# Kernel optimization log

Measured on AMD Instinct MI355X. Metric: run time of the kernel, lower is better.

Reference implementation:

```python
import jax, jax.numpy as jnp
import numpy as np

B, L, D, H, E, K = 1, 512, 512, 512, 32, 2

def setup_inputs() -> dict:
    key = jax.random.key(0)
    ks = jax.random.split(key, 6)
    x = jax.random.normal(ks[0], (B, L, D), dtype=jnp.float32)
    router_scale = 1.0 + 0.02 * jax.random.normal(ks[1], (D,), dtype=jnp.float32)
    router_logits_w = 0.02 * jax.random.normal(ks[2], (D, E), dtype=jnp.float32)
    gating_einsum = 0.02 * jax.random.normal(ks[3], (E, 2, H, D), dtype=jnp.float32)
    linear_w = 0.02 * jax.random.normal(ks[4], (E, H, D), dtype=jnp.float32)
    per_expert_scale = 1.0 + 0.02 * jax.random.normal(ks[5], (E,), dtype=jnp.float32)
    return {"x": x, "router_scale": router_scale, "router_logits_w": router_logits_w,
            "gating_einsum": gating_einsum, "linear_w": linear_w,
            "per_expert_scale": per_expert_scale}

def reference(x, router_scale, router_logits_w, gating_einsum, linear_w, per_expert_scale):
    d = x.shape[-1]
    n_experts = router_logits_w.shape[-1]
    # RMSNorm without scale (fp32)
    x32 = x.astype(jnp.float32)
    var = jnp.mean(jnp.square(x32), axis=-1, keepdims=True)
    router_input = x32 * jax.lax.rsqrt(var + 1e-6)
    root_size = jax.lax.rsqrt(jnp.asarray(d, dtype=router_input.dtype))
    router_input = router_input * root_size * router_scale.astype(router_input.dtype)
    logits = jnp.dot(router_input, router_logits_w).astype(jnp.float32)  # [B,L,E]
    probs = jax.nn.softmax(logits, axis=-1)
    _, top_k_indices = jax.lax.top_k(logits, K)  # [B,L,K]
    indicator = jax.nn.one_hot(top_k_indices, n_experts, dtype=probs.dtype).sum(axis=-2)
    gate_weights = indicator * probs
    renorm = jnp.sum(gate_weights, axis=-1, keepdims=True)
    renorm = jnp.where(renorm > 0.0, renorm, 1.0)
    weights = probs / renorm
    top_k_weights = jnp.take_along_axis(weights, top_k_indices, axis=-1)  # [B,L,K]
    output = jnp.zeros_like(x)
    for ki in range(K):  # small fixed k; faithful to source's per-slot gather
        expert_idx = top_k_indices[:, :, ki]          # [B,L] int32
        expert_w = top_k_weights[:, :, ki]            # [B,L]
        gate_params = gating_einsum[expert_idx]       # [B,L,2,H,D] -- the big gather
        lin_params = linear_w[expert_idx]             # [B,L,H,D]
        escale = per_expert_scale[expert_idx]         # [B,L]
        gate_0 = jnp.einsum('bld,blhd->blh', x, gate_params[:, :, 0])
        gate_1 = jnp.einsum('bld,blhd->blh', x, gate_params[:, :, 1])
        activated = jax.nn.gelu(gate_0) * gate_1
        expert_out = jnp.einsum('blh,blhd->bld', activated, lin_params)
        output = output + expert_out * (escale * expert_w)[..., None]
    return output
```

## Files before the change

### kernel.cpp

```cpp
#include <hip/hip_runtime.h>
#include <hip/hip_bf16.h>
#include <math.h>

#define LTOK 512
#define DDIM 512
#define NEXP 32
#define HDIM 512

typedef __attribute__((ext_vector_type(8))) short short8;
typedef __attribute__((ext_vector_type(4))) float floatx4;

__device__ __forceinline__ unsigned bpack(float a, float b) {
    unsigned ua = __float_as_uint(a), ub = __float_as_uint(b);
    ua += 0x7FFFu + ((ua >> 16) & 1u);
    ub += 0x7FFFu + ((ub >> 16) & 1u);
    return (ua >> 16) | (ub & 0xFFFF0000u);
}


__global__ __launch_bounds__(64) void router_kernel(
    const float* __restrict__ x, const float* __restrict__ rs,
    const float* __restrict__ Wr, const float* __restrict__ pes,
    int* __restrict__ cnt, int* __restrict__ alist, float* __restrict__ slist,
    short* __restrict__ xb)
{
    const int t = blockIdx.x;
    const int lane = threadIdx.x;

    float xv[8];
    float ss = 0.f;
#pragma unroll
    for (int j = 0; j < 8; ++j) {
        xv[j] = x[t * DDIM + j * 64 + lane];
        ss += xv[j] * xv[j];
    }
#pragma unroll
    for (int j = 0; j < 8; ++j)
        xb[t * DDIM + j * 64 + lane] = (short)(bpack(xv[j], 0.f) & 0xFFFFu);

#pragma unroll
    for (int o = 32; o > 0; o >>= 1) ss += __shfl_xor(ss, o);
    const float var = ss * (1.0f / 512.0f);
    const float coef = rsqrtf(var + 1e-6f) * rsqrtf(512.0f);

    __shared__ float ri[DDIM];
#pragma unroll
    for (int j = 0; j < 8; ++j) {
        const int d = j * 64 + lane;
        ri[d] = xv[j] * coef * rs[d];
    }
    __syncthreads();

    const int e = lane & 31;
    const int half = lane >> 5;
    const int dbeg = half * 256;
    float l0 = 0.f, l1 = 0.f, l2 = 0.f, l3 = 0.f;
#pragma unroll 4
    for (int d = dbeg; d < dbeg + 256; d += 4) {
        l0 = fmaf(ri[d + 0], Wr[(d + 0) * NEXP + e], l0);
        l1 = fmaf(ri[d + 1], Wr[(d + 1) * NEXP + e], l1);
        l2 = fmaf(ri[d + 2], Wr[(d + 2) * NEXP + e], l2);
        l3 = fmaf(ri[d + 3], Wr[(d + 3) * NEXP + e], l3);
    }
    float lg = (l0 + l1) + (l2 + l3);
    lg += __shfl_xor(lg, 32);

    __shared__ float lgs[NEXP];
    if (lane < 32) lgs[lane] = lg;
    __syncthreads();

    if (lane == 0) {
        int i0 = 0; float m0 = lgs[0];
        for (int i = 1; i < NEXP; ++i) if (lgs[i] > m0) { m0 = lgs[i]; i0 = i; }
        int i1 = -1; float m1 = -1e30f;
        for (int i = 0; i < NEXP; ++i) if (i != i0 && lgs[i] > m1) { m1 = lgs[i]; i1 = i; }
        const float e1 = expf(m1 - m0);
        const float inv = 1.0f / (1.0f + e1);
        const float w0 = inv, w1 = e1 * inv;

        int p0 = atomicAdd(&cnt[i0], 1);
        alist[i0 * LTOK + p0] = t * 2;
        slist[i0 * LTOK + p0] = w0 * pes[i0];
        int p1 = atomicAdd(&cnt[i1], 1);
        alist[i1 * LTOK + p1] = t * 2 + 1;
        slist[i1 * LTOK + p1] = w1 * pes[i1];
    }
}

__global__ __launch_bounds__(256, 4) void gates_kernel(
    const short* __restrict__ xb, const float* __restrict__ G,
    const int* __restrict__ cnt, const int* __restrict__ alist,
    short* __restrict__ act)
{
    const int e  = blockIdx.y;
    const int h0 = blockIdx.x * 16;
    const int Ne = cnt[e];
    if (Ne == 0) return;
    const int wv   = threadIdx.x >> 6;
    const int g    = wv & 1;
    const int kh   = wv >> 1;
    const int lane = threadIdx.x & 63;
    const int n    = lane & 15;
    const int quad = lane >> 4;

    __shared__ float red[4][4][4][64];

    const float* Grow = G + ((size_t)((e * 2 + g) * HDIM) + h0 + n) * DDIM + kh * 256;
    const short* xbh  = xb + kh * 256;
    const int* al = alist + e * LTOK;

    for (int mb = 0; mb < Ne; mb += 64) {
        int arow[4];
#pragma unroll
        for (int i = 0; i < 4; ++i) {
            int s = mb + i * 16 + n;
            arow[i] = al[s < Ne ? s : Ne - 1] >> 1;
        }
        floatx4 acc[4] = {};

#pragma unroll 4
        for (int ks = 0; ks < 8; ++ks) {
            const int ko = ks * 32 + quad * 8;
            const floatx4 b0 = *(const floatx4*)(Grow + ko);
            const floatx4 b1 = *(const floatx4*)(Grow + ko + 4);
            union { short8 s; unsigned u[4]; } B;
            B.u[0] = bpack(b0.x, b0.y);
            B.u[1] = bpack(b0.z, b0.w);
            B.u[2] = bpack(b1.x, b1.y);
            B.u[3] = bpack(b1.z, b1.w);
#pragma unroll
            for (int i = 0; i < 4; ++i) {
                const short8 A = *(const short8*)(xbh + (size_t)arow[i] * DDIM + ko);
                acc[i] = __builtin_amdgcn_mfma_f32_16x16x32_bf16(A, B.s, acc[i], 0, 0, 0);
            }
        }

#pragma unroll
        for (int i = 0; i < 4; ++i)
#pragma unroll
            for (int r = 0; r < 4; ++r)
                red[wv][i][r][lane] = acc[i][r];
        __syncthreads();

        {
            const int i = wv;
#pragma unroll
            for (int r = 0; r < 4; ++r) {
                const int s = mb + i * 16 + quad * 4 + r;
                if (s < Ne) {
                    const int a = al[s];
                    const float g0 = red[0][i][r][lane] + red[2][i][r][lane];
                    const float g1 = red[1][i][r][lane] + red[3][i][r][lane];
                    const float u = 0.7978845608f * (g0 + 0.044715f * g0 * g0 * g0);
                    const float sg = 1.0f / (1.0f + __expf(-2.0f * u));
                    const float v = g0 * sg * g1;
                    act[(size_t)a * HDIM + h0 + n] = (short)(bpack(v, 0.f) & 0xFFFFu);
                }
            }
        }
        __syncthreads();
    }
}

__global__ __launch_bounds__(256, 4) void linear_kernel(
    const short* __restrict__ act, const float* __restrict__ Wl,
    const int* __restrict__ cnt, const int* __restrict__ alist,
    const float* __restrict__ slist, float* __restrict__ out)
{
    const int e  = blockIdx.y;
    const int d0 = blockIdx.x * 16;
    const int Ne = cnt[e];
    if (Ne == 0) return;
    const int wv   = threadIdx.x >> 6;
    const int lane = threadIdx.x & 63;
    const int n    = lane & 15;
    const int quad = lane >> 4;

    __shared__ float red[4][4][4][64];

    const float* Wcol = Wl + (size_t)e * HDIM * DDIM + d0 + n;
    const int* al = alist + e * LTOK;
    const float* sl = slist + e * LTOK;

    for (int mb = 0; mb < Ne; mb += 64) {
        int arow[4];
#pragma unroll
        for (int i = 0; i < 4; ++i) {
            int s = mb + i * 16 + n;
            arow[i] = al[s < Ne ? s : Ne - 1];
        }
        floatx4 acc[4] = {};

#pragma unroll 2
        for (int ks = 0; ks < 4; ++ks) {
            const int ko = wv * 128 + ks * 32 + quad * 8;
            float w[8];
#pragma unroll
            for (int j = 0; j < 8; ++j)
                w[j] = Wcol[(size_t)(ko + j) * DDIM];
            union { short8 s; unsigned u[4]; } B;
            B.u[0] = bpack(w[0], w[1]);
            B.u[1] = bpack(w[2], w[3]);
            B.u[2] = bpack(w[4], w[5]);
            B.u[3] = bpack(w[6], w[7]);
#pragma unroll
            for (int i = 0; i < 4; ++i) {
                const short8 A = *(const short8*)(act + (size_t)arow[i] * HDIM + ko);
                acc[i] = __builtin_amdgcn_mfma_f32_16x16x32_bf16(A, B.s, acc[i], 0, 0, 0);
            }
        }

#pragma unroll
        for (int i = 0; i < 4; ++i)
#pragma unroll
            for (int r = 0; r < 4; ++r)
                red[wv][i][r][lane] = acc[i][r];
        __syncthreads();

        {
            const int i = wv;
#pragma unroll
            for (int r = 0; r < 4; ++r) {
                const int s = mb + i * 16 + quad * 4 + r;
                if (s < Ne) {
                    const int a = al[s];
                    const float v = ((red[0][i][r][lane] + red[1][i][r][lane]) +
                                     (red[2][i][r][lane] + red[3][i][r][lane])) * sl[s];
                    atomicAdd(&out[(size_t)(a >> 1) * DDIM + d0 + n], v);
                }
            }
        }
        __syncthreads();
    }
}

extern "C" void kernel_launch(void* const* d_in, const int* in_sizes, int n_in,
                              void* d_out, int out_size, void* d_ws, size_t ws_size,
                              hipStream_t stream)
{
    const float* x   = (const float*)d_in[0];
    const float* rs  = (const float*)d_in[1];
    const float* Wr  = (const float*)d_in[2];
    const float* G   = (const float*)d_in[3];
    const float* Wl  = (const float*)d_in[4];
    const float* pes = (const float*)d_in[5];
    float* out = (float*)d_out;

    char* ws = (char*)d_ws;
    int*   cnt   = (int*)(ws);
    int*   alist = (int*)(ws + 256);
    float* slist = (float*)(ws + 256 + 65536);
    short* xb    = (short*)(ws + 131328);
    short* act   = (short*)(ws + 655616);

    hipMemsetAsync(cnt, 0, NEXP * sizeof(int), stream);
    hipMemsetAsync(out, 0, (size_t)out_size * sizeof(float), stream);

    router_kernel<<<dim3(LTOK), dim3(64), 0, stream>>>(x, rs, Wr, pes, cnt, alist, slist, xb);
    gates_kernel<<<dim3(32, NEXP), dim3(256), 0, stream>>>(xb, G, cnt, alist, act);
    linear_kernel<<<dim3(32, NEXP), dim3(256), 0, stream>>>(act, Wl, cnt, alist, slist, out);
}
```

Before: 165.4 us.

## Hoist expert weight fragments into registers and replace atomics with combine kernel

Both expert GEMM kernels now load and convert their bf16 weight fragments once, before the token loop, and keep them in registers across all token tiles instead of reloading them per tile. The token tile shrinks from 64 to 32 rows to keep register use down. The linear kernel writes each (token, slot) result to a scratch buffer rather than doing atomicAdd into the output, and a new combine kernel sums the two slots per token. This drops the output memset and atomic contention, at the cost of an extra launch and extra scratch traffic.

```diff
diff --git a/kernel.cpp b/kernel.cpp
--- a/kernel.cpp
+++ b/kernel.cpp
@@ -103,56 +103,65 @@
     const int n    = lane & 15;
     const int quad = lane >> 4;
 
-    __shared__ float red[4][4][4][64];
+    __shared__ float red[4][2][4][64];
 
     const float* Grow = G + ((size_t)((e * 2 + g) * HDIM) + h0 + n) * DDIM + kh * 256;
     const short* xbh  = xb + kh * 256;
     const int* al = alist + e * LTOK;
 
-    for (int mb = 0; mb < Ne; mb += 64) {
-        int arow[4];
-#pragma unroll
-        for (int i = 0; i < 4; ++i) {
+    short8 Bf[8];
+#pragma unroll
+    for (int ks = 0; ks < 8; ++ks) {
+        const int ko = ks * 32 + quad * 8;
+        const floatx4 b0 = *(const floatx4*)(Grow + ko);
+        const floatx4 b1 = *(const floatx4*)(Grow + ko + 4);
+        union { short8 s; unsigned u[4]; } B;
+        B.u[0] = bpack(b0.x, b0.y);
+        B.u[1] = bpack(b0.z, b0.w);
+        B.u[2] = bpack(b1.x, b1.y);
+        B.u[3] = bpack(b1.z, b1.w);
+        Bf[ks] = B.s;
+    }
+
+    for (int mb = 0; mb < Ne; mb += 32) {
+        int arow[2];
+#pragma unroll
+        for (int i = 0; i < 2; ++i) {
             int s = mb + i * 16 + n;
             arow[i] = al[s < Ne ? s : Ne - 1] >> 1;
         }
-        floatx4 acc[4] = {};
-
-#pragma unroll 4
+        floatx4 acc[2] = {};
+
+#pragma unroll
         for (int ks = 0; ks < 8; ++ks) {
             const int ko = ks * 32 + quad * 8;
-            const floatx4 b0 = *(const floatx4*)(Grow + ko);
-            const floatx4 b1 = *(const floatx4*)(Grow + ko + 4);
-            union { short8 s; unsigned u[4]; } B;
-            B.u[0] = bpack(b0.x, b0.y);
-            B.u[1] = bpack(b0.z, b0.w);
-            B.u[2] = bpack(b1.x, b1.y);
-            B.u[3] = bpack(b1.z, b1.w);
-#pragma unroll
-            for (int i = 0; i < 4; ++i) {
+#pragma unroll
+            for (int i = 0; i < 2; ++i) {
                 const short8 A = *(const short8*)(xbh + (size_t)arow[i] * DDIM + ko);
-                acc[i] = __builtin_amdgcn_mfma_f32_16x16x32_bf16(A, B.s, acc[i], 0, 0, 0);
-            }
-        }
-
-#pragma unroll
-        for (int i = 0; i < 4; ++i)
+                acc[i] = __builtin_amdgcn_mfma_f32_16x16x32_bf16(A, Bf[ks], acc[i], 0, 0, 0);
+            }
+        }
+
+#pragma unroll
+        for (int i = 0; i < 2; ++i)
 #pragma unroll
             for (int r = 0; r < 4; ++r)
                 red[wv][i][r][lane] = acc[i][r];
         __syncthreads();
 
         {
-            const int i = wv;
-#pragma unroll
-            for (int r = 0; r < 4; ++r) {
+            const int i = wv & 1;
+            const int u = wv >> 1;
+#pragma unroll
+            for (int rr = 0; rr < 2; ++rr) {
+                const int r = u * 2 + rr;
                 const int s = mb + i * 16 + quad * 4 + r;
                 if (s < Ne) {
                     const int a = al[s];
                     const float g0 = red[0][i][r][lane] + red[2][i][r][lane];
                     const float g1 = red[1][i][r][lane] + red[3][i][r][lane];
-                    const float u = 0.7978845608f * (g0 + 0.044715f * g0 * g0 * g0);
-                    const float sg = 1.0f / (1.0f + __expf(-2.0f * u));
+                    const float uu = 0.7978845608f * (g0 + 0.044715f * g0 * g0 * g0);
+                    const float sg = 1.0f / (1.0f + __expf(-2.0f * uu));
                     const float v = g0 * sg * g1;
                     act[(size_t)a * HDIM + h0 + n] = (short)(bpack(v, 0.f) & 0xFFFFu);
                 }
@@ -165,7 +174,7 @@
 __global__ __launch_bounds__(256, 4) void linear_kernel(
     const short* __restrict__ act, const float* __restrict__ Wl,
     const int* __restrict__ cnt, const int* __restrict__ alist,
-    const float* __restrict__ slist, float* __restrict__ out)
+    const float* __restrict__ slist, float* __restrict__ yb)
 {
     const int e  = blockIdx.y;
     const int d0 = blockIdx.x * 16;
@@ -176,62 +185,81 @@
     const int n    = lane & 15;
     const int quad = lane >> 4;
 
-    __shared__ float red[4][4][4][64];
+    __shared__ float red[4][2][4][64];
 
     const float* Wcol = Wl + (size_t)e * HDIM * DDIM + d0 + n;
     const int* al = alist + e * LTOK;
     const float* sl = slist + e * LTOK;
 
-    for (int mb = 0; mb < Ne; mb += 64) {
-        int arow[4];
-#pragma unroll
-        for (int i = 0; i < 4; ++i) {
+    short8 Bf[4];
+#pragma unroll
+    for (int ks = 0; ks < 4; ++ks) {
+        const int ko = wv * 128 + ks * 32 + quad * 8;
+        float w[8];
+#pragma unroll
+        for (int j = 0; j < 8; ++j)
+            w[j] = Wcol[(size_t)(ko + j) * DDIM];
+        union { short8 s; unsigned u[4]; } B;
+        B.u[0] = bpack(w[0], w[1]);
+        B.u[1] = bpack(w[2], w[3]);
+        B.u[2] = bpack(w[4], w[5]);
+        B.u[3] = bpack(w[6], w[7]);
+        Bf[ks] = B.s;
+    }
+
+    for (int mb = 0; mb < Ne; mb += 32) {
+        int arow[2];
+#pragma unroll
+        for (int i = 0; i < 2; ++i) {
             int s = mb + i * 16 + n;
             arow[i] = al[s < Ne ? s : Ne - 1];
         }
-        floatx4 acc[4] = {};
-
-#pragma unroll 2
+        floatx4 acc[2] = {};
+
+#pragma unroll
         for (int ks = 0; ks < 4; ++ks) {
             const int ko = wv * 128 + ks * 32 + quad * 8;
-            float w[8];
-#pragma unroll
-            for (int j = 0; j < 8; ++j)
-                w[j] = Wcol[(size_t)(ko + j) * DDIM];
-            union { short8 s; unsigned u[4]; } B;
-            B.u[0] = bpack(w[0], w[1]);
-            B.u[1] = bpack(w[2], w[3]);
-            B.u[2] = bpack(w[4], w[5]);
-            B.u[3] = bpack(w[6], w[7]);
-#pragma unroll
-            for (int i = 0; i < 4; ++i) {
+#pragma unroll
+            for (int i = 0; i < 2; ++i) {
                 const short8 A = *(const short8*)(act + (size_t)arow[i] * HDIM + ko);
-                acc[i] = __builtin_amdgcn_mfma_f32_16x16x32_bf16(A, B.s, acc[i], 0, 0, 0);
-            }
-        }
-
-#pragma unroll
-        for (int i = 0; i < 4; ++i)
+                acc[i] = __builtin_amdgcn_mfma_f32_16x16x32_bf16(A, Bf[ks], acc[i], 0, 0, 0);
+            }
+        }
+
+#pragma unroll
+        for (int i = 0; i < 2; ++i)
 #pragma unroll
             for (int r = 0; r < 4; ++r)
                 red[wv][i][r][lane] = acc[i][r];
         __syncthreads();
 
         {
-            const int i = wv;
-#pragma unroll
-            for (int r = 0; r < 4; ++r) {
+            const int i = wv & 1;
+            const int u = wv >> 1;
+#pragma unroll
+            for (int rr = 0; rr < 2; ++rr) {
+                const int r = u * 2 + rr;
                 const int s = mb + i * 16 + quad * 4 + r;
                 if (s < Ne) {
                     const int a = al[s];
                     const float v = ((red[0][i][r][lane] + red[1][i][r][lane]) +
                                      (red[2][i][r][lane] + red[3][i][r][lane])) * sl[s];
-                    atomicAdd(&out[(size_t)(a >> 1) * DDIM + d0 + n], v);
+                    yb[(size_t)a * DDIM + d0 + n] = v;
                 }
             }
         }
         __syncthreads();
     }
+}
+
+__global__ __launch_bounds__(256) void combine_kernel(
+    const float* __restrict__ yb, float* __restrict__ out)
+{
+    const int idx = blockIdx.x * 256 + threadIdx.x;
+    const int t = idx >> 7, c = idx & 127;
+    const floatx4 a = ((const floatx4*)(yb + (size_t)(2 * t) * DDIM))[c];
+    const floatx4 b = ((const floatx4*)(yb + (size_t)(2 * t + 1) * DDIM))[c];
+    ((floatx4*)(out + (size_t)t * DDIM))[c] = a + b;
 }
 
 extern "C" void kernel_launch(void* const* d_in, const int* in_sizes, int n_in,
@@ -252,11 +280,12 @@
     float* slist = (float*)(ws + 256 + 65536);
     short* xb    = (short*)(ws + 131328);
     short* act   = (short*)(ws + 655616);
+    float* yb    = (float*)(ws + 1704192);
 
     hipMemsetAsync(cnt, 0, NEXP * sizeof(int), stream);
-    hipMemsetAsync(out, 0, (size_t)out_size * sizeof(float), stream);
 
     router_kernel<<<dim3(LTOK), dim3(64), 0, stream>>>(x, rs, Wr, pes, cnt, alist, slist, xb);
     gates_kernel<<<dim3(32, NEXP), dim3(256), 0, stream>>>(xb, G, cnt, alist, act);
-    linear_kernel<<<dim3(32, NEXP), dim3(256), 0, stream>>>(act, Wl, cnt, alist, slist, out);
-}
+    linear_kernel<<<dim3(32, NEXP), dim3(256), 0, stream>>>(act, Wl, cnt, alist, slist, yb);
+    combine_kernel<<<dim3(256), dim3(256), 0, stream>>>(yb, out);
+}
```

Result: no change. 167.1 us (+1.0%).
